# Kernel optimization log

Measured on AMD Instinct MI355X. Metric: run time of the kernel, lower is better.

The kernel has to match this reference:

```python
import jax, jax.numpy as jnp
import numpy as np

B, T, N, IN, H, P = 1, 48, 4096, 2, 64, 12


def _normalize_adj(adj):
    A = adj + jnp.eye(adj.shape[0], dtype=adj.dtype)
    d = jnp.sum(A, axis=1)
    dinv = jnp.where(d > 0, d ** -0.5, 0.0)
    return (dinv[:, None] * A) * dinv[None, :]


def _cell(inp, h, c, A, gcWi, gcbi, gcWh, gcbh, liWi, libi, liWh, libh):
    # graph conv: spmm(A, inp @ W) + bias, plus plain linears; all produce [BN, 4H]
    comb = (A @ (inp @ gcWi) + gcbi
            + A @ (h @ gcWh) + gcbh
            + inp @ liWi + libi
            + h @ liWh + libh)
    i_g, f_g, o_g, g_g = jnp.split(comb, 4, axis=1)
    new_c = jax.nn.sigmoid(f_g) * c + jax.nn.sigmoid(i_g) * jnp.tanh(g_g)
    new_h = jax.nn.sigmoid(o_g) * jnp.tanh(new_c)
    return new_h, new_c


def setup_inputs() -> dict:
    key = jax.random.key(0)
    ks = jax.random.split(key, 24)
    s_in = 1.0 / np.sqrt(4 * H)

    def p(k, shape):
        return jax.random.normal(k, shape, dtype=jnp.float32) * s_in

    adj = (jax.random.uniform(ks[1], (N, N)) < 0.01).astype(jnp.float32)
    return {
        "x": jax.random.normal(ks[0], (B, T, N * IN), dtype=jnp.float32),
        "adj": adj,
        "gcWi0": p(ks[2], (IN, 4 * H)), "gcbi0": p(ks[3], (4 * H,)),
        "gcWh0": p(ks[4], (H, 4 * H)), "gcbh0": p(ks[5], (4 * H,)),
        "liWi0": p(ks[6], (IN, 4 * H)), "libi0": p(ks[7], (4 * H,)),
        "liWh0": p(ks[8], (H, 4 * H)), "libh0": p(ks[9], (4 * H,)),
        "gcWi1": p(ks[10], (H, 4 * H)), "gcbi1": p(ks[11], (4 * H,)),
        "gcWh1": p(ks[12], (H, 4 * H)), "gcbh1": p(ks[13], (4 * H,)),
        "liWi1": p(ks[14], (H, 4 * H)), "libi1": p(ks[15], (4 * H,)),
        "liWh1": p(ks[16], (H, 4 * H)), "libh1": p(ks[17], (4 * H,)),
        "outW": p(ks[18], (H, P)), "outb": p(ks[19], (P,)),
    }


def reference(x, adj, gcWi0, gcbi0, gcWh0, gcbh0, liWi0, libi0, liWh0, libh0,
              gcWi1, gcbi1, gcWh1, gcbh1, liWi1, libi1, liWh1, libh1, outW, outb):
    A = _normalize_adj(adj)
    # [B,T,N*IN] -> time-major [T, B*N, IN]
    xs = x.reshape(B, T, N, IN).transpose(1, 0, 2, 3).reshape(T, B * N, IN)
    z = jnp.zeros((B * N, H), dtype=x.dtype)

    def step(carry, xt):
        h0, c0, h1, c1 = carry
        h0, c0 = _cell(xt, h0, c0, A, gcWi0, gcbi0, gcWh0, gcbh0,
                       liWi0, libi0, liWh0, libh0)
        # dropout is identity in eval mode
        h1, c1 = _cell(h0, h1, c1, A, gcWi1, gcbi1, gcWh1, gcbh1,
                       liWi1, libi1, liWh1, libh1)
        return (h0, c0, h1, c1), None

    (h0, c0, h1, c1), _ = jax.lax.scan(step, (z, z, z, z), xs)
    out = h1 @ outW + outb  # [B*N, P]
    return out.reshape(B, N, P)
```

## Files before the change

### kernel.cpp

```cpp
#include <hip/hip_runtime.h>
#include <math.h>

#define NN 4096
#define TT 48
#define HH 64
#define GG 256
#define PP 12
#define CAP 192
#define NH (NN * HH)

__device__ __forceinline__ float bcast_f(float v, int lane) {
  return __int_as_float(__builtin_amdgcn_readlane(__float_as_int(v), lane));
}
__device__ __forceinline__ int bcast_i(int v, int lane) {
  return __builtin_amdgcn_readlane(v, lane);
}

__launch_bounds__(256)
__global__ void k_prep(const float* gcbi0, const float* gcbh0,
                       const float* libi0, const float* libh0,
                       const float* gcbi1, const float* gcbh1,
                       const float* libi1, const float* libh1,
                       const float* gcWh0, const float* liWh0,
                       const float* gcWi1, const float* liWi1,
                       const float* gcWh1, const float* liWh1,
                       const float* gcWi0, const float* liWi0,
                       float* state, float4* Wg0, float4* Wg1,
                       float4* biasg0, float4* biasg1, float4* xq0) {
  int idx = blockIdx.x * 256 + threadIdx.x;
  int stride = gridDim.x * 256;
  for (int i = idx; i < 6 * NH; i += stride) state[i] = 0.0f;
  for (int i = idx; i < 64 * 2 * 64; i += stride) {
    int j = i & 63, m = (i >> 6) & 1, k = i >> 7;
    const float* W = m ? liWh0 : gcWh0;
    Wg0[i] = make_float4(W[k * GG + j], W[k * GG + j + 64],
                         W[k * GG + j + 128], W[k * GG + j + 192]);
  }
  for (int i = idx; i < 64 * 4 * 64; i += stride) {
    int j = i & 63, m = (i >> 6) & 3, k = i >> 8;
    const float* W = (m == 0) ? gcWi1 : (m == 1) ? liWi1 : (m == 2) ? gcWh1 : liWh1;
    Wg1[i] = make_float4(W[k * GG + j], W[k * GG + j + 64],
                         W[k * GG + j + 128], W[k * GG + j + 192]);
  }
  if (idx < 64) {
    int j = idx;
    biasg0[j] = make_float4(
        gcbi0[j] + gcbh0[j] + libi0[j] + libh0[j],
        gcbi0[j + 64] + gcbh0[j + 64] + libi0[j + 64] + libh0[j + 64],
        gcbi0[j + 128] + gcbh0[j + 128] + libi0[j + 128] + libh0[j + 128],
        gcbi0[j + 192] + gcbh0[j + 192] + libi0[j + 192] + libh0[j + 192]);
    biasg1[j] = make_float4(
        gcbi1[j] + gcbh1[j] + libi1[j] + libh1[j],
        gcbi1[j + 64] + gcbh1[j + 64] + libi1[j + 64] + libh1[j + 64],
        gcbi1[j + 128] + gcbh1[j + 128] + libi1[j + 128] + libh1[j + 128],
        gcbi1[j + 192] + gcbh1[j + 192] + libi1[j + 192] + libh1[j + 192]);
  } else if (idx < 320) {
    int i = idx - 64;
    int j = i & 63, m = i >> 6;
    const float* W = (m < 2) ? gcWi0 : liWi0;
    int kk = m & 1;
    xq0[i] = make_float4(W[kk * GG + j], W[kk * GG + j + 64],
                         W[kk * GG + j + 128], W[kk * GG + j + 192]);
  }
}

__launch_bounds__(256)
__global__ void k_build(const float* adj, float* dinv,
                        int* ell_col, float* ell_val, int* ell_cnt) {
  int r = blockIdx.x;
  __shared__ int cnt;
  __shared__ float red[256];
  if (threadIdx.x == 0) cnt = 0;
  __syncthreads();
  const float* row = adj + (size_t)r * NN;
  float s = 0.0f;
  for (int c = threadIdx.x; c < NN; c += 256) {
    float a = row[c];
    if (c == r) a += 1.0f;
    s += a;
    if (a != 0.0f) {
      int pos = atomicAdd(&cnt, 1);
      if (pos < CAP) {
        ell_col[(size_t)r * CAP + pos] = c;
        ell_val[(size_t)r * CAP + pos] = a;
      }
    }
  }
  red[threadIdx.x] = s;
  __syncthreads();
  for (int st = 128; st > 0; st >>= 1) {
    if (threadIdx.x < st) red[threadIdx.x] += red[threadIdx.x + st];
    __syncthreads();
  }
  int n = cnt < CAP ? cnt : CAP;
  for (int j = n + (int)threadIdx.x; j < CAP; j += 256) {
    ell_col[(size_t)r * CAP + j] = 0;
    ell_val[(size_t)r * CAP + j] = 0.0f;
  }
  if (threadIdx.x == 0) {
    int npad = (n + 7) & ~7;
    if (npad > CAP) npad = CAP;
    ell_cnt[r] = npad;
    dinv[r] = 1.0f / sqrtf(red[0]);
  }
}

__launch_bounds__(256)
__global__ void k_scale(const float* dinv, const int* ell_col, float* ell_val) {
  int idx = blockIdx.x * 256 + threadIdx.x;
  int r = idx / CAP;
  if (r >= NN) return;
  float v = ell_val[idx];
  if (v != 0.0f) ell_val[idx] = v * dinv[r] * dinv[ell_col[idx]];
}

__launch_bounds__(256)
__global__ void k_gax(const float* x, const int* ell_col, const float* ell_val,
                      const int* ell_cnt, float* gax) {
  int t = blockIdx.x >> 3;
  int seg = blockIdx.x & 7;
  __shared__ float xs[NN * 2];
  const float* xt = x + (size_t)t * NN * 2;
  for (int i = threadIdx.x; i < NN * 2; i += 256) xs[i] = xt[i];
  __syncthreads();
  int base = seg * 512 * 2;
  for (int oo = threadIdx.x; oo < 512 * 2; oo += 256) {
    int o = base + oo;
    int r = o >> 1, cmp = o & 1;
    int cnt = ell_cnt[r];
    const int* cp = ell_col + (size_t)r * CAP;
    const float* vp = ell_val + (size_t)r * CAP;
    float acc = 0.0f;
    for (int j = 0; j < cnt; j += 4) {
      acc += vp[j]     * xs[cp[j]     * 2 + cmp];
      acc += vp[j + 1] * xs[cp[j + 1] * 2 + cmp];
      acc += vp[j + 2] * xs[cp[j + 2] * 2 + cmp];
      acc += vp[j + 3] * xs[cp[j + 3] * 2 + cmp];
    }
    gax[(size_t)t * NN * 2 + o] = acc;
  }
}

__device__ __forceinline__ void cell0_body(
    int blk,
    const int* __restrict__ ell_col, const float* __restrict__ ell_val,
    const int* __restrict__ ell_cnt,
    const float2* __restrict__ Pr, float* __restrict__ Pw,
    float* __restrict__ c0,
    const float* __restrict__ xt, const float* __restrict__ gaxt,
    const float4* __restrict__ Wg0, const float4* __restrict__ biasg0,
    const float4* __restrict__ xq0) {
  const int tid = threadIdx.x;
  const int wave = tid >> 6, lane = tid & 63;
  const int r0 = blk * 8 + wave * 2;

  int myc[2][3]; float myv[2][3]; int cnts[2];
#pragma unroll
  for (int rr = 0; rr < 2; rr++) {
    int r = r0 + rr;
    cnts[rr] = ell_cnt[r];
#pragma unroll
    for (int chk = 0; chk < 3; chk++) {
      myc[rr][chk] = ell_col[(size_t)r * CAP + chk * 64 + lane];
      myv[rr][chk] = ell_val[(size_t)r * CAP + chk * 64 + lane];
    }
  }
  float gacc[2], hl[2];
#pragma unroll
  for (int rr = 0; rr < 2; rr++) {
    int cnt = cnts[rr];
    float acc = 0.0f;
#pragma unroll
    for (int chk = 0; chk < 3; chk++) {
      int base = chk * 64;
      if (base < cnt) {
        int lim = cnt - base; if (lim > 64) lim = 64;
        int mc = myc[rr][chk]; float mv = myv[rr][chk];
        for (int m = 0; m < lim; m += 8) {
          float2 ld[8]; float vv[8];
#pragma unroll
          for (int i = 0; i < 8; i++) {
            int cc = bcast_i(mc, m + i);
            vv[i] = bcast_f(mv, m + i);
            ld[i] = Pr[(size_t)cc * 64 + lane];
          }
#pragma unroll
          for (int i = 0; i < 8; i++) acc += vv[i] * ld[i].x;
        }
      }
    }
    gacc[rr] = acc;
    hl[rr] = Pr[(size_t)(r0 + rr) * 64 + lane].x;
  }

  float4 acc[2];
  {
    float4 b = biasg0[lane];
    float4 qg0 = xq0[lane], qg1 = xq0[64 + lane];
    float4 ql0 = xq0[128 + lane], ql1 = xq0[192 + lane];
#pragma unroll
    for (int rr = 0; rr < 2; rr++) {
      float xx0 = xt[(size_t)(r0 + rr) * 2];
      float xx1 = xt[(size_t)(r0 + rr) * 2 + 1];
      float gg0 = gaxt[(size_t)(r0 + rr) * 2];
      float gg1 = gaxt[(size_t)(r0 + rr) * 2 + 1];
      acc[rr].x = b.x + gg0 * qg0.x + gg1 * qg1.x + xx0 * ql0.x + xx1 * ql1.x;
      acc[rr].y = b.y + gg0 * qg0.y + gg1 * qg1.y + xx0 * ql0.y + xx1 * ql1.y;
      acc[rr].z = b.z + gg0 * qg0.z + gg1 * qg1.z + xx0 * ql0.z + xx1 * ql1.z;
      acc[rr].w = b.w + gg0 * qg0.w + gg1 * qg1.w + xx0 * ql0.w + xx1 * ql1.w;
    }
  }

  const float4* bw = Wg0 + lane;
#pragma unroll 4
  for (int k = 0; k < 64; k++) {
    float4 w0 = bw[(k * 2 + 0) * 64];
    float4 w1 = bw[(k * 2 + 1) * 64];
#pragma unroll
    for (int rr = 0; rr < 2; rr++) {
      float a0 = bcast_f(gacc[rr], k);
      float a1 = bcast_f(hl[rr], k);
      acc[rr].x += a0 * w0.x + a1 * w1.x;
      acc[rr].y += a0 * w0.y + a1 * w1.y;
      acc[rr].z += a0 * w0.z + a1 * w1.z;
      acc[rr].w += a0 * w0.w + a1 * w1.w;
    }
  }

#pragma unroll
  for (int rr = 0; rr < 2; rr++) {
    size_t gi = (size_t)(r0 + rr) * HH + lane;
    float cprev = c0[gi];
    float si = 1.0f / (1.0f + __expf(-acc[rr].x));
    float sf = 1.0f / (1.0f + __expf(-acc[rr].y));
    float so = 1.0f / (1.0f + __expf(-acc[rr].z));
    float cn = sf * cprev + si * tanhf(acc[rr].w);
    float hn = so * tanhf(cn);
    c0[gi] = cn;
    Pw[gi * 2 + 0] = hn;
  }
}

__device__ __forceinline__ void cell1_body(
    int blk,
    const int* __restrict__ ell_col, const float* __restrict__ ell_val,
    const int* __restrict__ ell_cnt,
    const float2* __restrict__ Pr, float* __restrict__ Pw,
    float* __restrict__ c1,
    const float4* __restrict__ Wg1, const float4* __restrict__ biasg1) {
  const int tid = threadIdx.x;
  const int wave = tid >> 6, lane = tid & 63;
  const int r0 = blk * 8 + wave * 2;

  int myc[2][3]; float myv[2][3]; int cnts[2];
#pragma unroll
  for (int rr = 0; rr < 2; rr++) {
    int r = r0 + rr;
    cnts[rr] = ell_cnt[r];
#pragma unroll
    for (int chk = 0; chk < 3; chk++) {
      myc[rr][chk] = ell_col[(size_t)r * CAP + chk * 64 + lane];
      myv[rr][chk] = ell_val[(size_t)r * CAP + chk * 64 + lane];
    }
  }
  float ga0[2], ga1[2], hl0[2], hl1[2];
#pragma unroll
  for (int rr = 0; rr < 2; rr++) {
    int cnt = cnts[rr];
    float a0 = 0.0f, a1 = 0.0f;
#pragma unroll
    for (int chk = 0; chk < 3; chk++) {
      int base = chk * 64;
      if (base < cnt) {
        int lim = cnt - base; if (lim > 64) lim = 64;
        int mc = myc[rr][chk]; float mv = myv[rr][chk];
        for (int m = 0; m < lim; m += 8) {
          float2 ld[8]; float vv[8];
#pragma unroll
          for (int i = 0; i < 8; i++) {
            int cc = bcast_i(mc, m + i);
            vv[i] = bcast_f(mv, m + i);
            ld[i] = Pr[(size_t)cc * 64 + lane];
          }
#pragma unroll
          for (int i = 0; i < 8; i++) {
            a0 += vv[i] * ld[i].x;
            a1 += vv[i] * ld[i].y;
          }
        }
      }
    }
    ga0[rr] = a0;
    ga1[rr] = a1;
    float2 hh = Pr[(size_t)(r0 + rr) * 64 + lane];
    hl0[rr] = hh.x;
    hl1[rr] = hh.y;
  }

  float4 acc[2];
  {
    float4 b = biasg1[lane];
    acc[0] = b; acc[1] = b;
  }
  const float4* bw = Wg1 + lane;
#pragma unroll 4
  for (int k = 0; k < 64; k++) {
    float4 w0 = bw[(k * 4 + 0) * 64];
    float4 w1 = bw[(k * 4 + 1) * 64];
    float4 w2 = bw[(k * 4 + 2) * 64];
    float4 w3 = bw[(k * 4 + 3) * 64];
#pragma unroll
    for (int rr = 0; rr < 2; rr++) {
      float a0 = bcast_f(ga0[rr], k);
      float a1 = bcast_f(hl0[rr], k);
      float a2 = bcast_f(ga1[rr], k);
      float a3 = bcast_f(hl1[rr], k);
      acc[rr].x += a0 * w0.x + a1 * w1.x + a2 * w2.x + a3 * w3.x;
      acc[rr].y += a0 * w0.y + a1 * w1.y + a2 * w2.y + a3 * w3.y;
      acc[rr].z += a0 * w0.z + a1 * w1.z + a2 * w2.z + a3 * w3.z;
      acc[rr].w += a0 * w0.w + a1 * w1.w + a2 * w2.w + a3 * w3.w;
    }
  }

#pragma unroll
  for (int rr = 0; rr < 2; rr++) {
    size_t gi = (size_t)(r0 + rr) * HH + lane;
    float cprev = c1[gi];
    float si = 1.0f / (1.0f + __expf(-acc[rr].x));
    float sf = 1.0f / (1.0f + __expf(-acc[rr].y));
    float so = 1.0f / (1.0f + __expf(-acc[rr].z));
    float cn = sf * cprev + si * tanhf(acc[rr].w);
    float hn = so * tanhf(cn);
    c1[gi] = cn;
    Pw[gi * 2 + 1] = hn;
  }
}

__launch_bounds__(256)
__global__ void k_cells(int c0blocks,
                        const int* __restrict__ ell_col,
                        const float* __restrict__ ell_val,
                        const int* __restrict__ ell_cnt,
                        const float2* __restrict__ Pr, float* __restrict__ Pw,
                        float* __restrict__ c0, float* __restrict__ c1,
                        const float* __restrict__ xt, const float* __restrict__ gaxt,
                        const float4* __restrict__ Wg0,
                        const float4* __restrict__ biasg0,
                        const float4* __restrict__ xq0,
                        const float4* __restrict__ Wg1,
                        const float4* __restrict__ biasg1) {
  int b = blockIdx.x;
  if (b < c0blocks) {
    cell0_body(b, ell_col, ell_val, ell_cnt, Pr, Pw, c0, xt, gaxt,
               Wg0, biasg0, xq0);
  } else {
    cell1_body(b - c0blocks, ell_col, ell_val, ell_cnt, Pr, Pw, c1,
               Wg1, biasg1);
  }
}

__launch_bounds__(256)
__global__ void k_out(const float* __restrict__ P0, const float* __restrict__ outW,
                      const float* __restrict__ outb, float* __restrict__ out) {
  int idx = blockIdx.x * 256 + threadIdx.x;
  if (idx >= NN * PP) return;
  int r = idx / PP, p = idx - r * PP;
  float acc = outb[p];
  const float* hrow = P0 + (size_t)r * 128;
#pragma unroll 16
  for (int k = 0; k < HH; k++) acc += hrow[k * 2 + 1] * outW[k * PP + p];
  out[idx] = acc;
}

extern "C" void kernel_launch(void* const* d_in, const int* in_sizes, int n_in,
                              void* d_out, int out_size, void* d_ws, size_t ws_size,
                              hipStream_t stream) {
  const float* x     = (const float*)d_in[0];
  const float* adj   = (const float*)d_in[1];
  const float* gcWi0 = (const float*)d_in[2];
  const float* gcbi0 = (const float*)d_in[3];
  const float* gcWh0 = (const float*)d_in[4];
  const float* gcbh0 = (const float*)d_in[5];
  const float* liWi0 = (const float*)d_in[6];
  const float* libi0 = (const float*)d_in[7];
  const float* liWh0 = (const float*)d_in[8];
  const float* libh0 = (const float*)d_in[9];
  const float* gcWi1 = (const float*)d_in[10];
  const float* gcbi1 = (const float*)d_in[11];
  const float* gcWh1 = (const float*)d_in[12];
  const float* gcbh1 = (const float*)d_in[13];
  const float* liWi1 = (const float*)d_in[14];
  const float* libi1 = (const float*)d_in[15];
  const float* liWh1 = (const float*)d_in[16];
  const float* libh1 = (const float*)d_in[17];
  const float* outW  = (const float*)d_in[18];
  const float* outb  = (const float*)d_in[19];

  char* ws = (char*)d_ws;
  size_t off = 0;
  auto carve = [&](size_t bytes) {
    void* p = ws + off;
    off += (bytes + 255) & ~(size_t)255;
    return p;
  };
  float*  dinv    = (float*)carve((size_t)NN * 4);
  int*    ell_col = (int*)carve((size_t)NN * CAP * 4);
  float*  ell_val = (float*)carve((size_t)NN * CAP * 4);
  int*    ell_cnt = (int*)carve((size_t)NN * 4);
  float*  state   = (float*)carve((size_t)6 * NH * 4);
  float*  gax     = (float*)carve((size_t)TT * NN * 2 * 4);
  float4* Wg0     = (float4*)carve((size_t)64 * 2 * 64 * 16);
  float4* Wg1     = (float4*)carve((size_t)64 * 4 * 64 * 16);
  float4* biasg0  = (float4*)carve((size_t)64 * 16);
  float4* biasg1  = (float4*)carve((size_t)64 * 16);
  float4* xq0     = (float4*)carve((size_t)256 * 16);

  float* P[2] = {state, state + 2 * NH};
  float* c0 = state + 4 * NH;
  float* c1 = state + 5 * NH;

  k_prep<<<512, 256, 0, stream>>>(gcbi0, gcbh0, libi0, libh0,
                                  gcbi1, gcbh1, libi1, libh1,
                                  gcWh0, liWh0, gcWi1, liWi1, gcWh1, liWh1,
                                  gcWi0, liWi0,
                                  state, Wg0, Wg1, biasg0, biasg1, xq0);
  k_build<<<NN, 256, 0, stream>>>(adj, dinv, ell_col, ell_val, ell_cnt);
  k_scale<<<(NN * CAP) / 256, 256, 0, stream>>>(dinv, ell_col, ell_val);
  k_gax<<<TT * 8, 256, 0, stream>>>(x, ell_col, ell_val, ell_cnt, gax);

  for (int k = 0; k <= TT; k++) {
    int A = k & 1;
    int c0blocks = (k < TT) ? NN / 8 : 0;
    int c1blocks = (k > 0) ? NN / 8 : 0;
    int grid = c0blocks + c1blocks;
    int tx = (k < TT) ? k : (TT - 1);
    k_cells<<<grid, 256, 0, stream>>>(
        c0blocks, ell_col, ell_val, ell_cnt,
        (const float2*)P[A ^ 1], P[A], c0, c1,
        x + (size_t)tx * NN * 2, gax + (size_t)tx * NN * 2,
        Wg0, biasg0, xq0, Wg1, biasg1);
  }

  k_out<<<(NN * PP + 255) / 256, 256, 0, stream>>>(P[0], outW, outb, (float*)d_out);
}
```

Measured before the change: 2.087 ms.

## Split cell GEMV K-dimension across wave pairs with LDS reduction

Doubles the block to 512 threads so each pair of waves handles the same two rows. Each wave in the pair computes half of the K=64 weight contraction, and the partial sums are combined through shared memory before the gate nonlinearities. The goal is to cut the serial per-wave dot-product latency and raise the number of waves in flight. The cost is that both waves redundantly do the sparse aggregation gather, and the change adds a __syncthreads and LDS traffic.

```diff
diff --git a/kernel.cpp b/kernel.cpp
--- a/kernel.cpp
+++ b/kernel.cpp
@@ -149,10 +149,11 @@
     float* __restrict__ c0,
     const float* __restrict__ xt, const float* __restrict__ gaxt,
     const float4* __restrict__ Wg0, const float4* __restrict__ biasg0,
-    const float4* __restrict__ xq0) {
+    const float4* __restrict__ xq0, float4* accred) {
   const int tid = threadIdx.x;
   const int wave = tid >> 6, lane = tid & 63;
-  const int r0 = blk * 8 + wave * 2;
+  const int pair = wave >> 1, kh = wave & 1;
+  const int r0 = blk * 8 + pair * 2;
 
   int myc[2][3]; float myv[2][3]; int cnts[2];
 #pragma unroll
@@ -194,7 +195,7 @@
   }
 
   float4 acc[2];
-  {
+  if (kh == 0) {
     float4 b = biasg0[lane];
     float4 qg0 = xq0[lane], qg1 = xq0[64 + lane];
     float4 ql0 = xq0[128 + lane], ql1 = xq0[192 + lane];
@@ -209,13 +210,18 @@
       acc[rr].z = b.z + gg0 * qg0.z + gg1 * qg1.z + xx0 * ql0.z + xx1 * ql1.z;
       acc[rr].w = b.w + gg0 * qg0.w + gg1 * qg1.w + xx0 * ql0.w + xx1 * ql1.w;
     }
-  }
-
-  const float4* bw = Wg0 + lane;
+  } else {
+    acc[0] = make_float4(0.0f, 0.0f, 0.0f, 0.0f);
+    acc[1] = make_float4(0.0f, 0.0f, 0.0f, 0.0f);
+  }
+
+  const int kbeg = kh * 32;
+  const float4* bw = Wg0 + lane + (size_t)kbeg * 2 * 64;
 #pragma unroll 4
-  for (int k = 0; k < 64; k++) {
-    float4 w0 = bw[(k * 2 + 0) * 64];
-    float4 w1 = bw[(k * 2 + 1) * 64];
+  for (int kk = 0; kk < 32; kk++) {
+    int k = kbeg + kk;
+    float4 w0 = bw[(kk * 2 + 0) * 64];
+    float4 w1 = bw[(kk * 2 + 1) * 64];
 #pragma unroll
     for (int rr = 0; rr < 2; rr++) {
       float a0 = bcast_f(gacc[rr], k);
@@ -227,17 +233,28 @@
     }
   }
 
-#pragma unroll
-  for (int rr = 0; rr < 2; rr++) {
-    size_t gi = (size_t)(r0 + rr) * HH + lane;
-    float cprev = c0[gi];
-    float si = 1.0f / (1.0f + __expf(-acc[rr].x));
-    float sf = 1.0f / (1.0f + __expf(-acc[rr].y));
-    float so = 1.0f / (1.0f + __expf(-acc[rr].z));
-    float cn = sf * cprev + si * tanhf(acc[rr].w);
-    float hn = so * tanhf(cn);
-    c0[gi] = cn;
-    Pw[gi * 2 + 0] = hn;
+  if (kh == 1) {
+#pragma unroll
+    for (int rr = 0; rr < 2; rr++)
+      accred[(pair * 2 + rr) * 64 + lane] = acc[rr];
+  }
+  __syncthreads();
+  if (kh == 0) {
+#pragma unroll
+    for (int rr = 0; rr < 2; rr++) {
+      float4 o = accred[(pair * 2 + rr) * 64 + lane];
+      float gx = acc[rr].x + o.x, gy = acc[rr].y + o.y;
+      float gz = acc[rr].z + o.z, gw = acc[rr].w + o.w;
+      size_t gi = (size_t)(r0 + rr) * HH + lane;
+      float cprev = c0[gi];
+      float si = 1.0f / (1.0f + __expf(-gx));
+      float sf = 1.0f / (1.0f + __expf(-gy));
+      float so = 1.0f / (1.0f + __expf(-gz));
+      float cn = sf * cprev + si * tanhf(gw);
+      float hn = so * tanhf(cn);
+      c0[gi] = cn;
+      Pw[gi * 2 + 0] = hn;
+    }
   }
 }
 
@@ -247,10 +264,12 @@
     const int* __restrict__ ell_cnt,
     const float2* __restrict__ Pr, float* __restrict__ Pw,
     float* __restrict__ c1,
-    const float4* __restrict__ Wg1, const float4* __restrict__ biasg1) {
+    const float4* __restrict__ Wg1, const float4* __restrict__ biasg1,
+    float4* accred) {
   const int tid = threadIdx.x;
   const int wave = tid >> 6, lane = tid & 63;
-  const int r0 = blk * 8 + wave * 2;
+  const int pair = wave >> 1, kh = wave & 1;
+  const int r0 = blk * 8 + pair * 2;
 
   int myc[2][3]; float myv[2][3]; int cnts[2];
 #pragma unroll
@@ -298,17 +317,23 @@
   }
 
   float4 acc[2];
-  {
+  if (kh == 0) {
     float4 b = biasg1[lane];
     acc[0] = b; acc[1] = b;
-  }
-  const float4* bw = Wg1 + lane;
+  } else {
+    acc[0] = make_float4(0.0f, 0.0f, 0.0f, 0.0f);
+    acc[1] = make_float4(0.0f, 0.0f, 0.0f, 0.0f);
+  }
+
+  const int kbeg = kh * 32;
+  const float4* bw = Wg1 + lane + (size_t)kbeg * 4 * 64;
 #pragma unroll 4
-  for (int k = 0; k < 64; k++) {
-    float4 w0 = bw[(k * 4 + 0) * 64];
-    float4 w1 = bw[(k * 4 + 1) * 64];
-    float4 w2 = bw[(k * 4 + 2) * 64];
-    float4 w3 = bw[(k * 4 + 3) * 64];
+  for (int kk = 0; kk < 32; kk++) {
+    int k = kbeg + kk;
+    float4 w0 = bw[(kk * 4 + 0) * 64];
+    float4 w1 = bw[(kk * 4 + 1) * 64];
+    float4 w2 = bw[(kk * 4 + 2) * 64];
+    float4 w3 = bw[(kk * 4 + 3) * 64];
 #pragma unroll
     for (int rr = 0; rr < 2; rr++) {
       float a0 = bcast_f(ga0[rr], k);
@@ -322,21 +347,32 @@
     }
   }
 
-#pragma unroll
-  for (int rr = 0; rr < 2; rr++) {
-    size_t gi = (size_t)(r0 + rr) * HH + lane;
-    float cprev = c1[gi];
-    float si = 1.0f / (1.0f + __expf(-acc[rr].x));
-    float sf = 1.0f / (1.0f + __expf(-acc[rr].y));
-    float so = 1.0f / (1.0f + __expf(-acc[rr].z));
-    float cn = sf * cprev + si * tanhf(acc[rr].w);
-    float hn = so * tanhf(cn);
-    c1[gi] = cn;
-    Pw[gi * 2 + 1] = hn;
-  }
-}
-
-__launch_bounds__(256)
+  if (kh == 1) {
+#pragma unroll
+    for (int rr = 0; rr < 2; rr++)
+      accred[(pair * 2 + rr) * 64 + lane] = acc[rr];
+  }
+  __syncthreads();
+  if (kh == 0) {
+#pragma unroll
+    for (int rr = 0; rr < 2; rr++) {
+      float4 o = accred[(pair * 2 + rr) * 64 + lane];
+      float gx = acc[rr].x + o.x, gy = acc[rr].y + o.y;
+      float gz = acc[rr].z + o.z, gw = acc[rr].w + o.w;
+      size_t gi = (size_t)(r0 + rr) * HH + lane;
+      float cprev = c1[gi];
+      float si = 1.0f / (1.0f + __expf(-gx));
+      float sf = 1.0f / (1.0f + __expf(-gy));
+      float so = 1.0f / (1.0f + __expf(-gz));
+      float cn = sf * cprev + si * tanhf(gw);
+      float hn = so * tanhf(cn);
+      c1[gi] = cn;
+      Pw[gi * 2 + 1] = hn;
+    }
+  }
+}
+
+__launch_bounds__(512, 8)
 __global__ void k_cells(int c0blocks,
                         const int* __restrict__ ell_col,
                         const float* __restrict__ ell_val,
@@ -349,13 +385,14 @@
                         const float4* __restrict__ xq0,
                         const float4* __restrict__ Wg1,
                         const float4* __restrict__ biasg1) {
+  __shared__ float4 accred[512];
   int b = blockIdx.x;
   if (b < c0blocks) {
     cell0_body(b, ell_col, ell_val, ell_cnt, Pr, Pw, c0, xt, gaxt,
-               Wg0, biasg0, xq0);
+               Wg0, biasg0, xq0, accred);
   } else {
     cell1_body(b - c0blocks, ell_col, ell_val, ell_cnt, Pr, Pw, c1,
-               Wg1, biasg1);
+               Wg1, biasg1, accred);
   }
 }
 
@@ -434,7 +471,7 @@
     int c1blocks = (k > 0) ? NN / 8 : 0;
     int grid = c0blocks + c1blocks;
     int tx = (k < TT) ? k : (TT - 1);
-    k_cells<<<grid, 256, 0, stream>>>(
+    k_cells<<<grid, 512, 0, stream>>>(
         c0blocks, ell_col, ell_val, ell_cnt,
         (const float2*)P[A ^ 1], P[A], c0, c1,
         x + (size_t)tx * NN * 2, gax + (size_t)tx * NN * 2,
```

Measured after the change: 2.613 ms. +25.2%, slower.

## Process eight rows per wave and co-schedule cell0/cell1 waves in one block

Applied to the files above, without the earlier changes.

Each wave now handles 8 rows instead of 2. The dense weight loop therefore loads each weight float4 once and reuses it across 8 rows, which cuts weight traffic per row. Blocks now cover 16 rows, with waves 0-1 running cell0 and waves 2-3 running cell1 on the same rows. The grid shrinks to NN/16 blocks, and at the first and last timestep half the waves sit idle. The cost is much higher register pressure (8 float4 accumulators plus the gathered values), fewer waves overall, and lower occupancy.

```diff
diff --git a/kernel.cpp b/kernel.cpp
--- a/kernel.cpp
+++ b/kernel.cpp
@@ -142,7 +142,7 @@
 }
 
 __device__ __forceinline__ void cell0_body(
-    int blk,
+    int r0, int lane,
     const int* __restrict__ ell_col, const float* __restrict__ ell_val,
     const int* __restrict__ ell_cnt,
     const float2* __restrict__ Pr, float* __restrict__ Pw,
@@ -150,56 +150,56 @@
     const float* __restrict__ xt, const float* __restrict__ gaxt,
     const float4* __restrict__ Wg0, const float4* __restrict__ biasg0,
     const float4* __restrict__ xq0) {
-  const int tid = threadIdx.x;
-  const int wave = tid >> 6, lane = tid & 63;
-  const int r0 = blk * 8 + wave * 2;
-
-  int myc[2][3]; float myv[2][3]; int cnts[2];
-#pragma unroll
-  for (int rr = 0; rr < 2; rr++) {
-    int r = r0 + rr;
-    cnts[rr] = ell_cnt[r];
-#pragma unroll
-    for (int chk = 0; chk < 3; chk++) {
-      myc[rr][chk] = ell_col[(size_t)r * CAP + chk * 64 + lane];
-      myv[rr][chk] = ell_val[(size_t)r * CAP + chk * 64 + lane];
-    }
-  }
-  float gacc[2], hl[2];
-#pragma unroll
-  for (int rr = 0; rr < 2; rr++) {
-    int cnt = cnts[rr];
-    float acc = 0.0f;
-#pragma unroll
-    for (int chk = 0; chk < 3; chk++) {
-      int base = chk * 64;
-      if (base < cnt) {
-        int lim = cnt - base; if (lim > 64) lim = 64;
-        int mc = myc[rr][chk]; float mv = myv[rr][chk];
-        for (int m = 0; m < lim; m += 8) {
-          float2 ld[8]; float vv[8];
-#pragma unroll
-          for (int i = 0; i < 8; i++) {
-            int cc = bcast_i(mc, m + i);
-            vv[i] = bcast_f(mv, m + i);
-            ld[i] = Pr[(size_t)cc * 64 + lane];
+  float gacc[8], hl[8];
+#pragma unroll
+  for (int pr = 0; pr < 4; pr++) {
+    int rbase = r0 + pr * 2;
+    int myc[2][3]; float myv[2][3]; int cnts[2];
+#pragma unroll
+    for (int rr = 0; rr < 2; rr++) {
+      int r = rbase + rr;
+      cnts[rr] = ell_cnt[r];
+#pragma unroll
+      for (int chk = 0; chk < 3; chk++) {
+        myc[rr][chk] = ell_col[(size_t)r * CAP + chk * 64 + lane];
+        myv[rr][chk] = ell_val[(size_t)r * CAP + chk * 64 + lane];
+      }
+    }
+#pragma unroll
+    for (int rr = 0; rr < 2; rr++) {
+      int cnt = cnts[rr];
+      float acc = 0.0f;
+#pragma unroll
+      for (int chk = 0; chk < 3; chk++) {
+        int base = chk * 64;
+        if (base < cnt) {
+          int lim = cnt - base; if (lim > 64) lim = 64;
+          int mc = myc[rr][chk]; float mv = myv[rr][chk];
+          for (int m = 0; m < lim; m += 8) {
+            float2 ld[8]; float vv[8];
+#pragma unroll
+            for (int i = 0; i < 8; i++) {
+              int cc = bcast_i(mc, m + i);
+              vv[i] = bcast_f(mv, m + i);
+              ld[i] = Pr[(size_t)cc * 64 + lane];
+            }
+#pragma unroll
+            for (int i = 0; i < 8; i++) acc += vv[i] * ld[i].x;
           }
-#pragma unroll
-          for (int i = 0; i < 8; i++) acc += vv[i] * ld[i].x;
         }
       }
-    }
-    gacc[rr] = acc;
-    hl[rr] = Pr[(size_t)(r0 + rr) * 64 + lane].x;
-  }
-
-  float4 acc[2];
+      gacc[pr * 2 + rr] = acc;
+      hl[pr * 2 + rr] = Pr[(size_t)(rbase + rr) * 64 + lane].x;
+    }
+  }
+
+  float4 acc[8];
   {
     float4 b = biasg0[lane];
     float4 qg0 = xq0[lane], qg1 = xq0[64 + lane];
     float4 ql0 = xq0[128 + lane], ql1 = xq0[192 + lane];
 #pragma unroll
-    for (int rr = 0; rr < 2; rr++) {
+    for (int rr = 0; rr < 8; rr++) {
       float xx0 = xt[(size_t)(r0 + rr) * 2];
       float xx1 = xt[(size_t)(r0 + rr) * 2 + 1];
       float gg0 = gaxt[(size_t)(r0 + rr) * 2];
@@ -212,12 +212,12 @@
   }
 
   const float4* bw = Wg0 + lane;
-#pragma unroll 4
+#pragma unroll 2
   for (int k = 0; k < 64; k++) {
     float4 w0 = bw[(k * 2 + 0) * 64];
     float4 w1 = bw[(k * 2 + 1) * 64];
 #pragma unroll
-    for (int rr = 0; rr < 2; rr++) {
+    for (int rr = 0; rr < 8; rr++) {
       float a0 = bcast_f(gacc[rr], k);
       float a1 = bcast_f(hl[rr], k);
       acc[rr].x += a0 * w0.x + a1 * w1.x;
@@ -228,7 +228,7 @@
   }
 
 #pragma unroll
-  for (int rr = 0; rr < 2; rr++) {
+  for (int rr = 0; rr < 8; rr++) {
     size_t gi = (size_t)(r0 + rr) * HH + lane;
     float cprev = c0[gi];
     float si = 1.0f / (1.0f + __expf(-acc[rr].x));
@@ -242,75 +242,77 @@
 }
 
 __device__ __forceinline__ void cell1_body(
-    int blk,
+    int r0, int lane,
     const int* __restrict__ ell_col, const float* __restrict__ ell_val,
     const int* __restrict__ ell_cnt,
     const float2* __restrict__ Pr, float* __restrict__ Pw,
     float* __restrict__ c1,
     const float4* __restrict__ Wg1, const float4* __restrict__ biasg1) {
-  const int tid = threadIdx.x;
-  const int wave = tid >> 6, lane = tid & 63;
-  const int r0 = blk * 8 + wave * 2;
-
-  int myc[2][3]; float myv[2][3]; int cnts[2];
-#pragma unroll
-  for (int rr = 0; rr < 2; rr++) {
-    int r = r0 + rr;
-    cnts[rr] = ell_cnt[r];
-#pragma unroll
-    for (int chk = 0; chk < 3; chk++) {
-      myc[rr][chk] = ell_col[(size_t)r * CAP + chk * 64 + lane];
-      myv[rr][chk] = ell_val[(size_t)r * CAP + chk * 64 + lane];
-    }
-  }
-  float ga0[2], ga1[2], hl0[2], hl1[2];
-#pragma unroll
-  for (int rr = 0; rr < 2; rr++) {
-    int cnt = cnts[rr];
-    float a0 = 0.0f, a1 = 0.0f;
-#pragma unroll
-    for (int chk = 0; chk < 3; chk++) {
-      int base = chk * 64;
-      if (base < cnt) {
-        int lim = cnt - base; if (lim > 64) lim = 64;
-        int mc = myc[rr][chk]; float mv = myv[rr][chk];
-        for (int m = 0; m < lim; m += 8) {
-          float2 ld[8]; float vv[8];
-#pragma unroll
-          for (int i = 0; i < 8; i++) {
-            int cc = bcast_i(mc, m + i);
-            vv[i] = bcast_f(mv, m + i);
-            ld[i] = Pr[(size_t)cc * 64 + lane];
-          }
-#pragma unroll
-          for (int i = 0; i < 8; i++) {
-            a0 += vv[i] * ld[i].x;
-            a1 += vv[i] * ld[i].y;
+  float ga0[8], ga1[8], hl0[8], hl1[8];
+#pragma unroll
+  for (int pr = 0; pr < 4; pr++) {
+    int rbase = r0 + pr * 2;
+    int myc[2][3]; float myv[2][3]; int cnts[2];
+#pragma unroll
+    for (int rr = 0; rr < 2; rr++) {
+      int r = rbase + rr;
+      cnts[rr] = ell_cnt[r];
+#pragma unroll
+      for (int chk = 0; chk < 3; chk++) {
+        myc[rr][chk] = ell_col[(size_t)r * CAP + chk * 64 + lane];
+        myv[rr][chk] = ell_val[(size_t)r * CAP + chk * 64 + lane];
+      }
+    }
+#pragma unroll
+    for (int rr = 0; rr < 2; rr++) {
+      int cnt = cnts[rr];
+      float a0 = 0.0f, a1 = 0.0f;
+#pragma unroll
+      for (int chk = 0; chk < 3; chk++) {
+        int base = chk * 64;
+        if (base < cnt) {
+          int lim = cnt - base; if (lim > 64) lim = 64;
+          int mc = myc[rr][chk]; float mv = myv[rr][chk];
+          for (int m = 0; m < lim; m += 8) {
+            float2 ld[8]; float vv[8];
+#pragma unroll
+            for (int i = 0; i < 8; i++) {
+              int cc = bcast_i(mc, m + i);
+              vv[i] = bcast_f(mv, m + i);
+              ld[i] = Pr[(size_t)cc * 64 + lane];
+            }
+#pragma unroll
+            for (int i = 0; i < 8; i++) {
+              a0 += vv[i] * ld[i].x;
+              a1 += vv[i] * ld[i].y;
+            }
           }
         }
       }
-    }
-    ga0[rr] = a0;
-    ga1[rr] = a1;
-    float2 hh = Pr[(size_t)(r0 + rr) * 64 + lane];
-    hl0[rr] = hh.x;
-    hl1[rr] = hh.y;
-  }
-
-  float4 acc[2];
+      ga0[pr * 2 + rr] = a0;
+      ga1[pr * 2 + rr] = a1;
+      float2 hh = Pr[(size_t)(rbase + rr) * 64 + lane];
+      hl0[pr * 2 + rr] = hh.x;
+      hl1[pr * 2 + rr] = hh.y;
+    }
+  }
+
+  float4 acc[8];
   {
     float4 b = biasg1[lane];
-    acc[0] = b; acc[1] = b;
-  }
+#pragma unroll
+    for (int rr = 0; rr < 8; rr++) acc[rr] = b;
+  }
+
   const float4* bw = Wg1 + lane;
-#pragma unroll 4
+#pragma unroll 2
   for (int k = 0; k < 64; k++) {
     float4 w0 = bw[(k * 4 + 0) * 64];
     float4 w1 = bw[(k * 4 + 1) * 64];
     float4 w2 = bw[(k * 4 + 2) * 64];
     float4 w3 = bw[(k * 4 + 3) * 64];
 #pragma unroll
-    for (int rr = 0; rr < 2; rr++) {
+    for (int rr = 0; rr < 8; rr++) {
       float a0 = bcast_f(ga0[rr], k);
       float a1 = bcast_f(hl0[rr], k);
       float a2 = bcast_f(ga1[rr], k);
@@ -323,7 +325,7 @@
   }
 
 #pragma unroll
-  for (int rr = 0; rr < 2; rr++) {
+  for (int rr = 0; rr < 8; rr++) {
     size_t gi = (size_t)(r0 + rr) * HH + lane;
     float cprev = c1[gi];
     float si = 1.0f / (1.0f + __expf(-acc[rr].x));
@@ -337,7 +339,7 @@
 }
 
 __launch_bounds__(256)
-__global__ void k_cells(int c0blocks,
+__global__ void k_cells(int c0on, int c1on,
                         const int* __restrict__ ell_col,
                         const float* __restrict__ ell_val,
                         const int* __restrict__ ell_cnt,
@@ -349,13 +351,18 @@
                         const float4* __restrict__ xq0,
                         const float4* __restrict__ Wg1,
                         const float4* __restrict__ biasg1) {
-  int b = blockIdx.x;
-  if (b < c0blocks) {
-    cell0_body(b, ell_col, ell_val, ell_cnt, Pr, Pw, c0, xt, gaxt,
-               Wg0, biasg0, xq0);
+  const int wave = threadIdx.x >> 6;
+  const int lane = threadIdx.x & 63;
+  const int wsub = wave & 1;
+  const int r0 = blockIdx.x * 16 + wsub * 8;
+  if (wave < 2) {
+    if (c0on)
+      cell0_body(r0, lane, ell_col, ell_val, ell_cnt, Pr, Pw, c0, xt, gaxt,
+                 Wg0, biasg0, xq0);
   } else {
-    cell1_body(b - c0blocks, ell_col, ell_val, ell_cnt, Pr, Pw, c1,
-               Wg1, biasg1);
+    if (c1on)
+      cell1_body(r0, lane, ell_col, ell_val, ell_cnt, Pr, Pw, c1,
+                 Wg1, biasg1);
   }
 }
 
@@ -430,12 +437,11 @@
 
   for (int k = 0; k <= TT; k++) {
     int A = k & 1;
-    int c0blocks = (k < TT) ? NN / 8 : 0;
-    int c1blocks = (k > 0) ? NN / 8 : 0;
-    int grid = c0blocks + c1blocks;
+    int c0on = (k < TT) ? 1 : 0;
+    int c1on = (k > 0) ? 1 : 0;
     int tx = (k < TT) ? k : (TT - 1);
-    k_cells<<<grid, 256, 0, stream>>>(
-        c0blocks, ell_col, ell_val, ell_cnt,
+    k_cells<<<NN / 16, 256, 0, stream>>>(
+        c0on, c1on, ell_col, ell_val, ell_cnt,
         (const float2*)P[A ^ 1], P[A], c0, c1,
         x + (size_t)tx * NN * 2, gax + (size_t)tx * NN * 2,
         Wg0, biasg0, xq0, Wg1, biasg1);
```

After: 2.900 ms. +38.9%, slower.
